# Kernel optimization log

Hardware: AMD Instinct MI355X
Metric: run time of the kernel (lower is better)

The kernel has to match this reference:

```python
import jax, jax.numpy as jnp
import numpy as np

D_MODEL = 768
N_HEAD = 12
BATCH = 2
SEQ = 2048
MASK_FILL = -100000.0


def setup_inputs() -> dict:
    key = jax.random.key(0)
    ks = jax.random.split(key, 10)
    s = 1.0 / np.sqrt(D_MODEL)
    inp = {
        "xEnc": jax.random.normal(ks[0], (BATCH, SEQ, D_MODEL), jnp.float32),
        "xDec": jax.random.normal(ks[1], (BATCH, SEQ, D_MODEL), jnp.float32),
        # causal mask: True where attention is disallowed (j > i)
        "mask": (jnp.arange(SEQ)[None, :] > jnp.arange(SEQ)[:, None])[None, None, :, :],
        "wQ": jax.random.uniform(ks[2], (D_MODEL, D_MODEL), jnp.float32, -s, s),
        "bQ": jax.random.uniform(ks[3], (D_MODEL,), jnp.float32, -s, s),
        "wK": jax.random.uniform(ks[4], (D_MODEL, D_MODEL), jnp.float32, -s, s),
        "bK": jax.random.uniform(ks[5], (D_MODEL,), jnp.float32, -s, s),
        "wV": jax.random.uniform(ks[6], (D_MODEL, D_MODEL), jnp.float32, -s, s),
        "bV": jax.random.uniform(ks[7], (D_MODEL,), jnp.float32, -s, s),
        "wOut": jax.random.uniform(ks[8], (D_MODEL, D_MODEL), jnp.float32, -s, s),
        "bOut": jax.random.uniform(ks[9], (D_MODEL,), jnp.float32, -s, s),
    }
    return inp


def reference(xEnc, xDec, mask, wQ, bQ, wK, bK, wV, bV, wOut, bOut):
    B, S, D = xEnc.shape
    H = N_HEAD
    Dh = D // H
    # torch Linear: y = x @ W.T + b
    Q = xDec @ wQ.T + bQ
    K = xEnc @ wK.T + bK
    V = xEnc @ wV.T + bV
    Q = Q.reshape(B, S, H, Dh).transpose(0, 2, 1, 3)  # [B,H,S,Dh]
    K = K.reshape(B, S, H, Dh).transpose(0, 2, 1, 3)
    V = V.reshape(B, S, H, Dh).transpose(0, 2, 1, 3)
    score = jnp.einsum("bhqd,bhkd->bhqk", Q, K) / jnp.sqrt(jnp.float32(Dh))
    score = jnp.where(mask, MASK_FILL, score)
    attn = jax.nn.softmax(score, axis=-1)
    ctx = jnp.einsum("bhqk,bhkd->bhqd", attn, V)  # [B,H,S,Dh]
    ctx = ctx.transpose(0, 2, 1, 3).reshape(B, S, D)
    return ctx @ wOut.T + bOut
```

## Files before the change

kernel.cpp:

```cpp
#include <hip/hip_runtime.h>
#include <stdint.h>
#include <stddef.h>

#define DMODEL 768
#define NHEAD 12
#define SEQLEN 2048
#define NBATCH 2
#define DH 64
#define MTOT (NBATCH*SEQLEN)

typedef short s16x4 __attribute__((ext_vector_type(4)));
typedef short s16x8 __attribute__((ext_vector_type(8)));
typedef float f32x4 __attribute__((ext_vector_type(4)));

#define XDECB_OFF 0u
#define XENCB_OFF 3145728u
#define WQB_OFF   6291456u
#define WKB_OFF   6881280u
#define WVB_OFF   7471104u
#define WOUTB_OFF 8060928u
#define QB_OFF    8650752u
#define KB_OFF    11796480u
#define VT_OFF    14942208u
#define CTXB_OFF  18087936u

#define QSCALE 0.18033688011112042f

static __device__ __forceinline__ unsigned short f2bf(float f) {
  union { float f; unsigned int u; } v; v.f = f;
  unsigned int r = v.u + 0x7fffu + ((v.u >> 16) & 1u);
  return (unsigned short)(r >> 16);
}

static __device__ __forceinline__ unsigned int pack2bf(float f0, float f1) {
  union { float f; unsigned int u; } a, b; a.f = f0; b.f = f1;
  return __builtin_amdgcn_perm(b.u + 0x8000u, a.u + 0x8000u, 0x07060302u);
}

#if __has_builtin(__builtin_amdgcn_exp2f)
#define EXP2(x) __builtin_amdgcn_exp2f(x)
#else
#define EXP2(x) exp2f(x)
#endif

static __device__ __forceinline__ f32x4 mfma16(s16x4 a, s16x4 b, f32x4 c) {
  return __builtin_amdgcn_mfma_f32_16x16x16bf16_1k(a, b, c, 0, 0, 0);
}
static __device__ __forceinline__ f32x4 mfma32(s16x8 a, s16x8 b, f32x4 c) {
  return __builtin_amdgcn_mfma_f32_16x16x32_bf16(a, b, c, 0, 0, 0);
}

typedef __attribute__((address_space(3))) unsigned int lds_u32_t;
typedef const __attribute__((address_space(1))) unsigned int glb_u32_t;
static __device__ __forceinline__ void gl_lds16(const unsigned short* g,
                                                unsigned short* l) {
  __builtin_amdgcn_global_load_lds((glb_u32_t*)g, (lds_u32_t*)l, 16, 0, 0);
}

__global__ __launch_bounds__(256) void cvt_kernel(
    const float* __restrict__ xDec, const float* __restrict__ xEnc,
    const float* __restrict__ wQ, const float* __restrict__ wK,
    const float* __restrict__ wV, const float* __restrict__ wOut,
    unsigned short* __restrict__ ws)
{
  const int seg = blockIdx.y;
  const float* src;
  unsigned int n4, off;
  switch (seg) {
    case 0:  src = xDec; n4 = 786432; off = XDECB_OFF; break;
    case 1:  src = xEnc; n4 = 786432; off = XENCB_OFF; break;
    case 2:  src = wQ;   n4 = 147456; off = WQB_OFF;   break;
    case 3:  src = wK;   n4 = 147456; off = WKB_OFF;   break;
    case 4:  src = wV;   n4 = 147456; off = WVB_OFF;   break;
    default: src = wOut; n4 = 147456; off = WOUTB_OFF; break;
  }
  unsigned short* d = ws + off;
  const unsigned int stride = gridDim.x * blockDim.x;
  for (unsigned int i = blockIdx.x * blockDim.x + threadIdx.x; i < n4; i += stride) {
    const float4 v = ((const float4*)src)[i];
    s16x4 p;
    p[0] = (short)f2bf(v.x); p[1] = (short)f2bf(v.y);
    p[2] = (short)f2bf(v.z); p[3] = (short)f2bf(v.w);
    ((s16x4*)d)[i] = p;
  }
}

#define BK 64

__global__ __launch_bounds__(256, 6) void qkv_gemm(
    const unsigned short* __restrict__ xDecB, const unsigned short* __restrict__ xEncB,
    const unsigned short* __restrict__ wQB, const unsigned short* __restrict__ wKB,
    const unsigned short* __restrict__ wVB,
    const float* __restrict__ bQ, const float* __restrict__ bK, const float* __restrict__ bV,
    unsigned short* __restrict__ Qb, unsigned short* __restrict__ Kb,
    unsigned short* __restrict__ Vt)
{
  const int z = blockIdx.z;
  const unsigned short* __restrict__ A = (z == 0) ? xDecB : xEncB;
  const unsigned short* __restrict__ B = (z == 0) ? wQB : ((z == 1) ? wKB : wVB);
  const float* __restrict__ bias = (z == 0) ? bQ : ((z == 1) ? bK : bV);

  __shared__ unsigned short lA[64 * BK];
  __shared__ unsigned short lB[64 * BK];

  const int tid  = threadIdx.x;
  const int lane = tid & 63;
  const int wid  = tid >> 6;
  const int ln   = lane & 15;
  const int qd   = lane >> 4;
  const int m0 = blockIdx.x * 64;
  const int n0 = blockIdx.y * 64;
  const int wm = (wid & 1) * 32;
  const int wn = (wid >> 1) * 32;

  int srow[2], scol[2];
  #pragma unroll
  for (int c = 0; c < 2; ++c) {
    const int s = c * 256 + wid * 64 + lane;
    srow[c] = s >> 3;
    scol[c] = (((s & 7) ^ ((s >> 3) & 7)) * 8);
  }

  f32x4 acc[2][2] = {};

  for (int k0 = 0; k0 < DMODEL; k0 += BK) {
    #pragma unroll
    for (int c = 0; c < 2; ++c) {
      const int ldsoff = (c * 256 + wid * 64) * 8;
      gl_lds16(A + (size_t)(m0 + srow[c]) * DMODEL + k0 + scol[c], &lA[ldsoff]);
      gl_lds16(B + (size_t)(n0 + srow[c]) * DMODEL + k0 + scol[c], &lB[ldsoff]);
    }
    __syncthreads();
    #pragma unroll
    for (int kc = 0; kc < 2; ++kc) {
      s16x8 af[2], bfr[2];
      #pragma unroll
      for (int i = 0; i < 2; ++i) {
        const int r = wm + i * 16 + ln;
        af[i] = *(const s16x8*)&lA[r * 64 + (((kc * 4 + qd) ^ (r & 7)) * 8)];
      }
      #pragma unroll
      for (int j = 0; j < 2; ++j) {
        const int r = wn + j * 16 + ln;
        bfr[j] = *(const s16x8*)&lB[r * 64 + (((kc * 4 + qd) ^ (r & 7)) * 8)];
      }
      #pragma unroll
      for (int i = 0; i < 2; ++i)
        #pragma unroll
        for (int j = 0; j < 2; ++j)
          acc[i][j] = mfma32(af[i], bfr[j], acc[i][j]);
    }
    __syncthreads();
  }

  #pragma unroll
  for (int j = 0; j < 2; ++j) {
    const int n_g = n0 + wn + j * 16 + ln;
    const float bv = bias[n_g];
    const int h    = n_g >> 6;
    const int dcol = n_g & 63;
    #pragma unroll
    for (int i = 0; i < 2; ++i) {
      #pragma unroll
      for (int r = 0; r < 4; ++r) {
        const int m_g  = m0 + wm + i * 16 + qd * 4 + r;
        const int bb   = m_g >> 11;
        const int srow2 = m_g & 2047;
        const float val = acc[i][j][r] + bv;
        if (z == 0)
          Qb[((size_t)((bb * NHEAD + h) * SEQLEN + srow2)) * DH + dcol] = f2bf(val * QSCALE);
        else if (z == 1)
          Kb[((size_t)((bb * NHEAD + h) * SEQLEN + srow2)) * DH + dcol] = f2bf(val);
        else
          Vt[((size_t)((bb * NHEAD + h) * DH + dcol)) * SEQLEN + srow2] = f2bf(val);
      }
    }
  }
}

__global__ __launch_bounds__(256, 6) void out_gemm(
    const unsigned short* __restrict__ ctx, const unsigned short* __restrict__ wOutB,
    const float* __restrict__ bOut, float* __restrict__ out)
{
  __shared__ unsigned short lA[64 * BK];
  __shared__ unsigned short lB[64 * BK];

  const int tid  = threadIdx.x;
  const int lane = tid & 63;
  const int wid  = tid >> 6;
  const int ln   = lane & 15;
  const int qd   = lane >> 4;
  const int m0 = blockIdx.x * 64;
  const int n0 = blockIdx.y * 64;
  const int wm = (wid & 1) * 32;
  const int wn = (wid >> 1) * 32;

  int srow[2], scol[2];
  #pragma unroll
  for (int c = 0; c < 2; ++c) {
    const int s = c * 256 + wid * 64 + lane;
    srow[c] = s >> 3;
    scol[c] = (((s & 7) ^ ((s >> 3) & 7)) * 8);
  }

  f32x4 acc[2][2] = {};

  for (int k0 = 0; k0 < DMODEL; k0 += BK) {
    #pragma unroll
    for (int c = 0; c < 2; ++c) {
      const int ldsoff = (c * 256 + wid * 64) * 8;
      gl_lds16(ctx + (size_t)(m0 + srow[c]) * DMODEL + k0 + scol[c], &lA[ldsoff]);
      gl_lds16(wOutB + (size_t)(n0 + srow[c]) * DMODEL + k0 + scol[c], &lB[ldsoff]);
    }
    __syncthreads();
    #pragma unroll
    for (int kc = 0; kc < 2; ++kc) {
      s16x8 af[2], bfr[2];
      #pragma unroll
      for (int i = 0; i < 2; ++i) {
        const int r = wm + i * 16 + ln;
        af[i] = *(const s16x8*)&lA[r * 64 + (((kc * 4 + qd) ^ (r & 7)) * 8)];
      }
      #pragma unroll
      for (int j = 0; j < 2; ++j) {
        const int r = wn + j * 16 + ln;
        bfr[j] = *(const s16x8*)&lB[r * 64 + (((kc * 4 + qd) ^ (r & 7)) * 8)];
      }
      #pragma unroll
      for (int i = 0; i < 2; ++i)
        #pragma unroll
        for (int j = 0; j < 2; ++j)
          acc[i][j] = mfma32(af[i], bfr[j], acc[i][j]);
    }
    __syncthreads();
  }

  #pragma unroll
  for (int j = 0; j < 2; ++j) {
    const int n_g = n0 + wn + j * 16 + ln;
    const float bv = bOut[n_g];
    #pragma unroll
    for (int i = 0; i < 2; ++i) {
      #pragma unroll
      for (int r = 0; r < 4; ++r) {
        const int m_g = m0 + wm + i * 16 + qd * 4 + r;
        out[(size_t)m_g * DMODEL + n_g] = acc[i][j][r] + bv;
      }
    }
  }
}

#define KVT 128
#define LKP 72
#define LVP 136

__global__ __launch_bounds__(256, 3) void attn_kernel(
    const unsigned short* __restrict__ Qb, const unsigned short* __restrict__ Kb,
    const unsigned short* __restrict__ Vt, unsigned short* __restrict__ ctx)
{
  __shared__ unsigned short lK[KVT * LKP];
  __shared__ unsigned short lV[DH * LVP];

  const int tid  = threadIdx.x;
  const int lane = tid & 63;
  const int wid  = tid >> 6;
  const int ln   = lane & 15;
  const int qd   = lane >> 4;
  const int bh = blockIdx.y;
  const int q0 = (gridDim.x - 1 - blockIdx.x) * 64;
  const int q_lane = q0 + wid * 16 + ln;

  s16x8 qf[2];
  {
    const unsigned short* Qrow = Qb + ((size_t)bh * SEQLEN + q_lane) * DH;
    qf[0] = *(const s16x8*)(Qrow + qd * 8);
    qf[1] = *(const s16x8*)(Qrow + 32 + qd * 8);
  }

  float l_run = 0.0f;
  f32x4 o_acc[4] = {};

  const unsigned short* Kbase = Kb + (size_t)bh * SEQLEN * DH;
  const unsigned short* Vbase = Vt + (size_t)bh * DH * SEQLEN;
  const int kv_end = q0 + 64;
  const int ntiles = (kv_end + KVT - 1) / KVT;

  s16x8 rK[4], rV[4];
  auto load_kv = [&](int kv0) {
    #pragma unroll
    for (int i = 0; i < 4; ++i) {
      const int f = tid + i * 256;
      rK[i] = *(const s16x8*)(Kbase + (size_t)(kv0 + (f >> 3)) * DH + (f & 7) * 8);
    }
    #pragma unroll
    for (int i = 0; i < 4; ++i) {
      const int f = tid + i * 256;
      rV[i] = *(const s16x8*)(Vbase + (size_t)(f >> 4) * SEQLEN + kv0 + (f & 15) * 8);
    }
  };

  load_kv(0);
  for (int t0 = 0; t0 < ntiles; ++t0) {
    const int kv0 = t0 * KVT;
    #pragma unroll
    for (int i = 0; i < 4; ++i) {
      const int f = tid + i * 256;
      *(s16x8*)&lK[(f >> 3) * LKP + (f & 7) * 8] = rK[i];
    }
    #pragma unroll
    for (int i = 0; i < 4; ++i) {
      const int f = tid + i * 256;
      *(s16x8*)&lV[(f >> 4) * LVP + (f & 15) * 8] = rV[i];
    }
    __syncthreads();
    if (t0 + 1 < ntiles) load_kv(kv0 + KVT);

    f32x4 s_acc[8] = {};
    #pragma unroll
    for (int kc = 0; kc < 2; ++kc) {
      #pragma unroll
      for (int t = 0; t < 8; ++t) {
        const s16x8 a = *(const s16x8*)&lK[(t * 16 + ln) * LKP + kc * 32 + qd * 8];
        s_acc[t] = mfma32(a, qf[kc], s_acc[t]);
      }
    }

    if (kv0 + KVT > q0) {
      #pragma unroll
      for (int t = 0; t < 8; ++t) {
        #pragma unroll
        for (int r = 0; r < 4; ++r) {
          const int kv = kv0 + t * 16 + qd * 4 + r;
          s_acc[t][r] = (kv > q_lane) ? -1e30f : s_acc[t][r];
        }
      }
    }

    s16x4 pf[8];
    #pragma unroll
    for (int t = 0; t < 8; ++t) {
      const float p0 = EXP2(s_acc[t][0]);
      const float p1 = EXP2(s_acc[t][1]);
      const float p2 = EXP2(s_acc[t][2]);
      const float p3 = EXP2(s_acc[t][3]);
      l_run += (p0 + p1) + (p2 + p3);
      union { unsigned int u[2]; s16x4 v; } pk;
      pk.u[0] = pack2bf(p0, p1);
      pk.u[1] = pack2bf(p2, p3);
      pf[t] = pk.v;
    }

    #pragma unroll
    for (int t = 0; t < 8; ++t) {
      #pragma unroll
      for (int j = 0; j < 4; ++j) {
        const s16x4 b = *(const s16x4*)&lV[(j * 16 + ln) * LVP + t * 16 + qd * 4];
        o_acc[j] = mfma16(pf[t], b, o_acc[j]);
      }
    }
    __syncthreads();
  }

  l_run += __shfl_xor(l_run, 16);
  l_run += __shfl_xor(l_run, 32);

  const int bb = bh / NHEAD;
  const int h  = bh % NHEAD;
  #pragma unroll
  for (int r = 0; r < 4; ++r) {
    const float lr  = __shfl(l_run, qd * 4 + r);
    const float inv = 1.0f / lr;
    const int q_g = q0 + wid * 16 + qd * 4 + r;
    unsigned short* dst = ctx + ((size_t)bb * SEQLEN + q_g) * DMODEL + h * DH;
    #pragma unroll
    for (int j = 0; j < 4; ++j)
      dst[j * 16 + ln] = f2bf(o_acc[j][r] * inv);
  }
}

extern "C" void kernel_launch(void* const* d_in, const int* in_sizes, int n_in,
                              void* d_out, int out_size, void* d_ws, size_t ws_size,
                              hipStream_t stream)
{
  const float* xEnc = (const float*)d_in[0];
  const float* xDec = (const float*)d_in[1];
  const float* wQ   = (const float*)d_in[3];
  const float* bQ   = (const float*)d_in[4];
  const float* wK   = (const float*)d_in[5];
  const float* bK   = (const float*)d_in[6];
  const float* wV   = (const float*)d_in[7];
  const float* bV   = (const float*)d_in[8];
  const float* wOut = (const float*)d_in[9];
  const float* bOut = (const float*)d_in[10];

  unsigned short* ws = (unsigned short*)d_ws;

  cvt_kernel<<<dim3(512, 6), 256, 0, stream>>>(xDec, xEnc, wQ, wK, wV, wOut, ws);
  qkv_gemm<<<dim3(MTOT / 64, DMODEL / 64, 3), 256, 0, stream>>>(
      ws + XDECB_OFF, ws + XENCB_OFF, ws + WQB_OFF, ws + WKB_OFF, ws + WVB_OFF,
      bQ, bK, bV, ws + QB_OFF, ws + KB_OFF, ws + VT_OFF);
  attn_kernel<<<dim3(SEQLEN / 64, NBATCH * NHEAD), 256, 0, stream>>>(
      ws + QB_OFF, ws + KB_OFF, ws + VT_OFF, ws + CTXB_OFF);
  out_gemm<<<dim3(MTOT / 64, DMODEL / 64), 256, 0, stream>>>(
      ws + CTXB_OFF, ws + WOUTB_OFF, bOut, (float*)d_out);
}
```

Before: 190.9 us.

## Balance causal attention work by pairing query tiles and splitting long KV ranges

```diff
diff --git a/kernel.cpp b/kernel.cpp
--- a/kernel.cpp
+++ b/kernel.cpp
@@ -256,7 +256,9 @@
 
 __global__ __launch_bounds__(256, 3) void attn_kernel(
     const unsigned short* __restrict__ Qb, const unsigned short* __restrict__ Kb,
-    const unsigned short* __restrict__ Vt, unsigned short* __restrict__ ctx)
+    const unsigned short* __restrict__ Vt, unsigned short* __restrict__ ctx,
+    float* __restrict__ pout0, float* __restrict__ pout1,
+    float* __restrict__ lpart)
 {
   __shared__ unsigned short lK[KVT * LKP];
   __shared__ unsigned short lV[DH * LVP];
@@ -267,115 +269,163 @@
   const int ln   = lane & 15;
   const int qd   = lane >> 4;
   const int bh = blockIdx.y;
-  const int q0 = (gridDim.x - 1 - blockIdx.x) * 64;
-  const int q_lane = q0 + wid * 16 + ln;
-
-  s16x8 qf[2];
-  {
-    const unsigned short* Qrow = Qb + ((size_t)bh * SEQLEN + q_lane) * DH;
-    qf[0] = *(const s16x8*)(Qrow + qd * 8);
-    qf[1] = *(const s16x8*)(Qrow + 32 + qd * 8);
-  }
-
-  float l_run = 0.0f;
-  f32x4 o_acc[4] = {};
+  const int p  = blockIdx.x;
+  const bool isA = p < 16;
+  const int i  = isA ? p : (p - 16);
+  const int Ti = (i + 2) >> 1;
 
   const unsigned short* Kbase = Kb + (size_t)bh * SEQLEN * DH;
   const unsigned short* Vbase = Vt + (size_t)bh * DH * SEQLEN;
-  const int kv_end = q0 + 64;
-  const int ntiles = (kv_end + KVT - 1) / KVT;
-
-  s16x8 rK[4], rV[4];
-  auto load_kv = [&](int kv0) {
-    #pragma unroll
-    for (int i = 0; i < 4; ++i) {
-      const int f = tid + i * 256;
-      rK[i] = *(const s16x8*)(Kbase + (size_t)(kv0 + (f >> 3)) * DH + (f & 7) * 8);
-    }
-    #pragma unroll
-    for (int i = 0; i < 4; ++i) {
-      const int f = tid + i * 256;
-      rV[i] = *(const s16x8*)(Vbase + (size_t)(f >> 4) * SEQLEN + kv0 + (f & 15) * 8);
-    }
-  };
-
-  load_kv(0);
-  for (int t0 = 0; t0 < ntiles; ++t0) {
-    const int kv0 = t0 * KVT;
-    #pragma unroll
-    for (int i = 0; i < 4; ++i) {
-      const int f = tid + i * 256;
-      *(s16x8*)&lK[(f >> 3) * LKP + (f & 7) * 8] = rK[i];
-    }
-    #pragma unroll
-    for (int i = 0; i < 4; ++i) {
-      const int f = tid + i * 256;
-      *(s16x8*)&lV[(f >> 4) * LVP + (f & 15) * 8] = rV[i];
-    }
-    __syncthreads();
-    if (t0 + 1 < ntiles) load_kv(kv0 + KVT);
-
-    f32x4 s_acc[8] = {};
-    #pragma unroll
-    for (int kc = 0; kc < 2; ++kc) {
-      #pragma unroll
-      for (int t = 0; t < 8; ++t) {
-        const s16x8 a = *(const s16x8*)&lK[(t * 16 + ln) * LKP + kc * 32 + qd * 8];
-        s_acc[t] = mfma32(a, qf[kc], s_acc[t]);
-      }
-    }
-
-    if (kv0 + KVT > q0) {
-      #pragma unroll
-      for (int t = 0; t < 8; ++t) {
-        #pragma unroll
-        for (int r = 0; r < 4; ++r) {
-          const int kv = kv0 + t * 16 + qd * 4 + r;
-          s_acc[t][r] = (kv > q_lane) ? -1e30f : s_acc[t][r];
-        }
-      }
-    }
-
-    s16x4 pf[8];
-    #pragma unroll
-    for (int t = 0; t < 8; ++t) {
-      const float p0 = EXP2(s_acc[t][0]);
-      const float p1 = EXP2(s_acc[t][1]);
-      const float p2 = EXP2(s_acc[t][2]);
-      const float p3 = EXP2(s_acc[t][3]);
-      l_run += (p0 + p1) + (p2 + p3);
-      union { unsigned int u[2]; s16x4 v; } pk;
-      pk.u[0] = pack2bf(p0, p1);
-      pk.u[1] = pack2bf(p2, p3);
-      pf[t] = pk.v;
-    }
-
-    #pragma unroll
-    for (int t = 0; t < 8; ++t) {
-      #pragma unroll
-      for (int j = 0; j < 4; ++j) {
-        const s16x4 b = *(const s16x4*)&lV[(j * 16 + ln) * LVP + t * 16 + qd * 4];
-        o_acc[j] = mfma16(pf[t], b, o_acc[j]);
-      }
-    }
-    __syncthreads();
-  }
-
-  l_run += __shfl_xor(l_run, 16);
-  l_run += __shfl_xor(l_run, 32);
-
   const int bb = bh / NHEAD;
   const int h  = bh % NHEAD;
-  #pragma unroll
-  for (int r = 0; r < 4; ++r) {
-    const float lr  = __shfl(l_run, qd * 4 + r);
-    const float inv = 1.0f / lr;
-    const int q_g = q0 + wid * 16 + qd * 4 + r;
-    unsigned short* dst = ctx + ((size_t)bb * SEQLEN + q_g) * DMODEL + h * DH;
-    #pragma unroll
-    for (int j = 0; j < 4; ++j)
-      dst[j * 16 + ln] = f2bf(o_acc[j][r] * inv);
-  }
+
+  auto run = [&](int q0, int t0, int nt, int mode) {
+    const int q_lane = q0 + wid * 16 + ln;
+    s16x8 qf[2];
+    {
+      const unsigned short* Qrow = Qb + ((size_t)bh * SEQLEN + q_lane) * DH;
+      qf[0] = *(const s16x8*)(Qrow + qd * 8);
+      qf[1] = *(const s16x8*)(Qrow + 32 + qd * 8);
+    }
+    float l_run = 0.0f;
+    f32x4 o_acc[4] = {};
+
+    s16x8 rK[4], rV[4];
+    auto load_kv = [&](int kv0) {
+      #pragma unroll
+      for (int c = 0; c < 4; ++c) {
+        const int f = tid + c * 256;
+        rK[c] = *(const s16x8*)(Kbase + (size_t)(kv0 + (f >> 3)) * DH + (f & 7) * 8);
+      }
+      #pragma unroll
+      for (int c = 0; c < 4; ++c) {
+        const int f = tid + c * 256;
+        rV[c] = *(const s16x8*)(Vbase + (size_t)(f >> 4) * SEQLEN + kv0 + (f & 15) * 8);
+      }
+    };
+
+    load_kv(t0 * KVT);
+    for (int t = t0; t < t0 + nt; ++t) {
+      const int kv0 = t * KVT;
+      #pragma unroll
+      for (int c = 0; c < 4; ++c) {
+        const int f = tid + c * 256;
+        *(s16x8*)&lK[(f >> 3) * LKP + (f & 7) * 8] = rK[c];
+      }
+      #pragma unroll
+      for (int c = 0; c < 4; ++c) {
+        const int f = tid + c * 256;
+        *(s16x8*)&lV[(f >> 4) * LVP + (f & 15) * 8] = rV[c];
+      }
+      __syncthreads();
+      if (t + 1 < t0 + nt) load_kv(kv0 + KVT);
+
+      f32x4 s_acc[8] = {};
+      #pragma unroll
+      for (int kc = 0; kc < 2; ++kc) {
+        #pragma unroll
+        for (int t8 = 0; t8 < 8; ++t8) {
+          const s16x8 a = *(const s16x8*)&lK[(t8 * 16 + ln) * LKP + kc * 32 + qd * 8];
+          s_acc[t8] = mfma32(a, qf[kc], s_acc[t8]);
+        }
+      }
+
+      if (kv0 + KVT > q0) {
+        #pragma unroll
+        for (int t8 = 0; t8 < 8; ++t8) {
+          #pragma unroll
+          for (int r = 0; r < 4; ++r) {
+            const int kv = kv0 + t8 * 16 + qd * 4 + r;
+            s_acc[t8][r] = (kv > q_lane) ? -1e30f : s_acc[t8][r];
+          }
+        }
+      }
+
+      s16x4 pf[8];
+      #pragma unroll
+      for (int t8 = 0; t8 < 8; ++t8) {
+        const float p0 = EXP2(s_acc[t8][0]);
+        const float p1 = EXP2(s_acc[t8][1]);
+        const float p2 = EXP2(s_acc[t8][2]);
+        const float p3 = EXP2(s_acc[t8][3]);
+        l_run += (p0 + p1) + (p2 + p3);
+        union { unsigned int u[2]; s16x4 v; } pk;
+        pk.u[0] = pack2bf(p0, p1);
+        pk.u[1] = pack2bf(p2, p3);
+        pf[t8] = pk.v;
+      }
+
+      #pragma unroll
+      for (int t8 = 0; t8 < 8; ++t8) {
+        #pragma unroll
+        for (int j = 0; j < 4; ++j) {
+          const s16x4 b = *(const s16x4*)&lV[(j * 16 + ln) * LVP + t8 * 16 + qd * 4];
+          o_acc[j] = mfma16(pf[t8], b, o_acc[j]);
+        }
+      }
+      __syncthreads();
+    }
+
+    l_run += __shfl_xor(l_run, 16);
+    l_run += __shfl_xor(l_run, 32);
+
+    if (mode == 0) {
+      #pragma unroll
+      for (int r = 0; r < 4; ++r) {
+        const float lr  = __shfl(l_run, qd * 4 + r);
+        const float inv = 1.0f / lr;
+        const int q_g = q0 + wid * 16 + qd * 4 + r;
+        unsigned short* dst = ctx + ((size_t)bb * SEQLEN + q_g) * DMODEL + h * DH;
+        #pragma unroll
+        for (int j = 0; j < 4; ++j)
+          dst[j * 16 + ln] = f2bf(o_acc[j][r] * inv);
+      }
+    } else {
+      float* PO = (mode == 1) ? pout1 : pout0;
+      float* LO = lpart + ((mode == 1) ? (24 * 1024) : 0);
+      const int qbase = q0 - 1024 + wid * 16;
+      if (lane < 16)
+        LO[bh * 1024 + qbase + lane] = l_run;
+      #pragma unroll
+      for (int j = 0; j < 4; ++j)
+        #pragma unroll
+        for (int r = 0; r < 4; ++r)
+          PO[((size_t)bh * 1024 + qbase + qd * 4 + r) * 64 + j * 16 + ln] =
+              o_acc[j][r];
+    }
+  };
+
+  if (isA) {
+    run(i * 64, 0, Ti, 0);
+    run((31 - i) * 64, 0, 9 - Ti, 1);
+  } else {
+    run((31 - i) * 64, 9 - Ti, 8, 2);
+  }
+}
+
+__global__ __launch_bounds__(256) void norm_kernel(
+    const float* __restrict__ pout0, const float* __restrict__ pout1,
+    const float* __restrict__ lpart, unsigned short* __restrict__ ctx)
+{
+  const int e4  = blockIdx.x * 256 + threadIdx.x;
+  const int d4  = e4 & 15;
+  const int row = e4 >> 4;
+  const int bh  = row >> 10;
+  const int qr  = row & 1023;
+  const float l = lpart[row] + lpart[24 * 1024 + row];
+  const float inv = 1.0f / l;
+  const float4 a = ((const float4*)pout0)[e4];
+  const float4 b = ((const float4*)pout1)[e4];
+  const int bb = bh / NHEAD;
+  const int h  = bh % NHEAD;
+  unsigned short* dst =
+      ctx + ((size_t)bb * SEQLEN + 1024 + qr) * DMODEL + h * DH + d4 * 4;
+  s16x4 o;
+  o[0] = (short)f2bf((a.x + b.x) * inv);
+  o[1] = (short)f2bf((a.y + b.y) * inv);
+  o[2] = (short)f2bf((a.z + b.z) * inv);
+  o[3] = (short)f2bf((a.w + b.w) * inv);
+  *(s16x4*)dst = o;
 }
 
 extern "C" void kernel_launch(void* const* d_in, const int* in_sizes, int n_in,
@@ -394,13 +444,19 @@
   const float* bOut = (const float*)d_in[10];
 
   unsigned short* ws = (unsigned short*)d_ws;
+  float* pout0 = (float*)(ws + XDECB_OFF);
+  float* pout1 = (float*)(ws + XENCB_OFF);
+  float* lpart = (float*)(ws + WQB_OFF);
 
   cvt_kernel<<<dim3(512, 6), 256, 0, stream>>>(xDec, xEnc, wQ, wK, wV, wOut, ws);
   qkv_gemm<<<dim3(MTOT / 64, DMODEL / 64, 3), 256, 0, stream>>>(
       ws + XDECB_OFF, ws + XENCB_OFF, ws + WQB_OFF, ws + WKB_OFF, ws + WVB_OFF,
       bQ, bK, bV, ws + QB_OFF, ws + KB_OFF, ws + VT_OFF);
-  attn_kernel<<<dim3(SEQLEN / 64, NBATCH * NHEAD), 256, 0, stream>>>(
-      ws + QB_OFF, ws + KB_OFF, ws + VT_OFF, ws + CTXB_OFF);
+  attn_kernel<<<dim3(32, NBATCH * NHEAD), 256, 0, stream>>>(
+      ws + QB_OFF, ws + KB_OFF, ws + VT_OFF, ws + CTXB_OFF,
+      pout0, pout1, lpart);
+  norm_kernel<<<dim3((24 * 1024 * 16) / 256), 256, 0, stream>>>(
+      pout0, pout1, lpart, ws + CTXB_OFF);
   out_gemm<<<dim3(MTOT / 64, DMODEL / 64), 256, 0, stream>>>(
       ws + CTXB_OFF, ws + WOUTB_OFF, bOut, (float*)d_out);
 }
```

New measurement: 184.1 us. 3.6% less time.
